# Kernel tuning notes

Hardware: AMD Instinct MI355X
Metric: run time of the kernel (lower is better)

The kernel has to match this reference:

```python
import jax, jax.numpy as jnp
import numpy as np
import math

D_MODEL = 512
N_HEADS = 8
D_K = D_MODEL // N_HEADS
B, S = 2, 4096
LN_EPS = 1e-5


def _xavier(key, fan_in, fan_out):
    limit = math.sqrt(6.0 / (fan_in + fan_out))
    return jax.random.uniform(key, (fan_in, fan_out), jnp.float32, -limit, limit)


def setup_inputs() -> dict:
    key = jax.random.key(0)
    ks = jax.random.split(key, 12)
    x = jax.random.normal(ks[0], (B, S, D_MODEL), jnp.float32)
    consciousness_state = jax.random.normal(ks[1], (B, D_MODEL), jnp.float32)
    # weights stored as [in, out] (equivalent to torch Linear weight.T)
    w_q = _xavier(ks[2], D_MODEL, D_MODEL)
    w_k = _xavier(ks[3], D_MODEL, D_MODEL)
    w_v = _xavier(ks[4], D_MODEL, D_MODEL)
    w_o = _xavier(ks[5], D_MODEL, D_MODEL)
    b_o = jnp.zeros((D_MODEL,), jnp.float32)
    w_gate = _xavier(ks[6], D_MODEL, N_HEADS)
    b_gate = jnp.zeros((N_HEADS,), jnp.float32)
    w_int = _xavier(ks[7], D_MODEL, D_MODEL)
    b_int = jnp.zeros((D_MODEL,), jnp.float32)
    ln_gamma = jnp.ones((D_MODEL,), jnp.float32)
    ln_beta = jnp.zeros((D_MODEL,), jnp.float32)
    return {"x": x, "consciousness_state": consciousness_state,
            "w_q": w_q, "w_k": w_k, "w_v": w_v, "w_o": w_o, "b_o": b_o,
            "w_gate": w_gate, "b_gate": b_gate, "w_int": w_int, "b_int": b_int,
            "ln_gamma": ln_gamma, "ln_beta": ln_beta}


def reference(x, consciousness_state, w_q, w_k, w_v, w_o, b_o,
              w_gate, b_gate, w_int, b_int, ln_gamma, ln_beta):
    b, s, d = x.shape
    # project and split heads: [B, H, S, d_k]
    def heads(w):
        return (x @ w).reshape(b, s, N_HEADS, D_K).transpose(0, 2, 1, 3)
    Q, K, V = heads(w_q), heads(w_k), heads(w_v)
    scores = jnp.einsum('bhsd,bhtd->bhst', Q, K) / math.sqrt(D_K)  # [B,H,S,S]
    # per-head consciousness gate BEFORE softmax
    cw = jax.nn.sigmoid(consciousness_state @ w_gate + b_gate)  # [B,H]
    scores = scores * cw[:, :, None, None]
    attn = jax.nn.softmax(scores, axis=-1)
    # dropout is identity in eval mode
    context = jnp.einsum('bhst,bhtd->bhsd', attn, V)
    context = context.transpose(0, 2, 1, 3).reshape(b, s, d)
    out = context @ w_o + b_o
    iw = jax.nn.sigmoid(consciousness_state @ w_int + b_int)  # [B,D]
    out = out * iw[:, None, :]
    # residual + LayerNorm
    h = out + x
    mu = jnp.mean(h, axis=-1, keepdims=True)
    var = jnp.var(h, axis=-1, keepdims=True)
    out = (h - mu) * jax.lax.rsqrt(var + LN_EPS) * ln_gamma + ln_beta
    return out, attn.mean(axis=1)
```

## Files before the change

### kernel.cpp

```cpp
#include <hip/hip_runtime.h>
#include <hip/hip_bf16.h>

using short8 = __attribute__((ext_vector_type(8))) short;
using f32x4  = __attribute__((ext_vector_type(4))) float;

#define S_LEN 4096
#define DM 512

__device__ __forceinline__ unsigned short f2b(float f) {
    unsigned int u = __float_as_uint(f);
    u += 0x7fffu + ((u >> 16) & 1u);
    return (unsigned short)(u >> 16);
}

__device__ __forceinline__ short8 pack8(float4 a, float4 b) {
    short8 r;
    r[0] = (short)f2b(a.x); r[1] = (short)f2b(a.y); r[2] = (short)f2b(a.z); r[3] = (short)f2b(a.w);
    r[4] = (short)f2b(b.x); r[5] = (short)f2b(b.y); r[6] = (short)f2b(b.z); r[7] = (short)f2b(b.w);
    return r;
}

__global__ __launch_bounds__(256) void convert_w(
    const float* __restrict__ w0, const float* __restrict__ w1,
    const float* __restrict__ w2, const float* __restrict__ w3,
    unsigned short* __restrict__ t0, unsigned short* __restrict__ t1,
    unsigned short* __restrict__ t2, unsigned short* __restrict__ t3)
{
    __shared__ float sh[64][65];
    const float* src; unsigned short* dst;
    switch (blockIdx.z) {
        case 0: src = w0; dst = t0; break;
        case 1: src = w1; dst = t1; break;
        case 2: src = w2; dst = t2; break;
        default: src = w3; dst = t3; break;
    }
    int k0 = blockIdx.x * 64, n0 = blockIdx.y * 64;
    int tid = threadIdx.x;
    for (int i = tid; i < 4096; i += 256) {
        int k = i >> 6, n = i & 63;
        sh[k][n] = src[(size_t)(k0 + k) * DM + n0 + n];
    }
    __syncthreads();
    for (int i = tid; i < 4096; i += 256) {
        int n = i >> 6, k = i & 63;
        dst[(size_t)(n0 + n) * DM + k0 + k] = f2b(sh[k][n]);
    }
}

__global__ __launch_bounds__(256) void convert_x(
    const float* __restrict__ x, unsigned short* __restrict__ xb)
{
    size_t i = ((size_t)blockIdx.x * 256 + threadIdx.x) * 8;
    float4 a = *reinterpret_cast<const float4*>(x + i);
    float4 b = *reinterpret_cast<const float4*>(x + i + 4);
    *reinterpret_cast<short8*>(xb + i) = pack8(a, b);
}

__global__ __launch_bounds__(64) void gates_kernel(
    const float* __restrict__ cs, const float* __restrict__ wg, const float* __restrict__ bg,
    const float* __restrict__ wi, const float* __restrict__ bi,
    float* __restrict__ cwout, float* __restrict__ iwout)
{
    int o = blockIdx.x, b = blockIdx.y, lane = threadIdx.x;
    const float* c = cs + (size_t)b * DM;
    float acc = 0.f;
    if (o < 8) {
        #pragma unroll
        for (int j = 0; j < 8; ++j) { int k = j * 64 + lane; acc += c[k] * wg[(size_t)k * 8 + o]; }
    } else {
        int n = o - 8;
        #pragma unroll
        for (int j = 0; j < 8; ++j) { int k = j * 64 + lane; acc += c[k] * wi[(size_t)k * DM + n]; }
    }
    #pragma unroll
    for (int d = 32; d; d >>= 1) acc += __shfl_xor(acc, d);
    if (lane == 0) {
        if (o < 8) cwout[b * 8 + o] = 1.f / (1.f + __expf(-(acc + bg[o])));
        else       iwout[b * DM + (o - 8)] = 1.f / (1.f + __expf(-(acc + bi[o - 8])));
    }
}

__global__ __launch_bounds__(256) void gemm_qkv(
    const unsigned short* __restrict__ A, const unsigned short* __restrict__ WT,
    const float* __restrict__ cw,
    unsigned short* __restrict__ Qb, unsigned short* __restrict__ Kb,
    unsigned short* __restrict__ Vt)
{
    __shared__ unsigned short a_sh[64][72];
    __shared__ unsigned short b_sh[64][72];
    const int m0 = blockIdx.x * 64;
    const int n0g = blockIdx.y * 64;
    const int which = blockIdx.y >> 3;
    const int tid = threadIdx.x;
    const int wave = tid >> 6, lane = tid & 63;
    const int g = lane >> 4, lr = lane & 15;
    const int srow = tid >> 3, skc = (tid & 7) * 8;

    float sq = 1.f;
    if (which == 0) {
        int b = blockIdx.x >> 6;
        int h = blockIdx.y & 7;
        sq = cw[b * 8 + h] * 0.125f * 1.44269504f;
    }

    f32x4 acc[4];
    #pragma unroll
    for (int i = 0; i < 4; ++i) acc[i] = (f32x4){0.f, 0.f, 0.f, 0.f};

    short8 ar[2], br[2];
    #pragma unroll
    for (int cc = 0; cc < 2; ++cc) {
        int row = srow + cc * 32;
        ar[cc] = *reinterpret_cast<const short8*>(A  + (size_t)(m0  + row) * DM + skc);
        br[cc] = *reinterpret_cast<const short8*>(WT + (size_t)(n0g + row) * DM + skc);
    }

    for (int k0 = 0; k0 < 512; k0 += 64) {
        #pragma unroll
        for (int cc = 0; cc < 2; ++cc) {
            int row = srow + cc * 32;
            *reinterpret_cast<short8*>(&a_sh[row][skc]) = ar[cc];
            *reinterpret_cast<short8*>(&b_sh[row][skc]) = br[cc];
        }
        __syncthreads();
        if (k0 + 64 < 512) {
            #pragma unroll
            for (int cc = 0; cc < 2; ++cc) {
                int row = srow + cc * 32;
                ar[cc] = *reinterpret_cast<const short8*>(A  + (size_t)(m0  + row) * DM + k0 + 64 + skc);
                br[cc] = *reinterpret_cast<const short8*>(WT + (size_t)(n0g + row) * DM + k0 + 64 + skc);
            }
        }
        __builtin_amdgcn_s_setprio(1);
        #pragma unroll
        for (int ks = 0; ks < 2; ++ks) {
            short8 af = *reinterpret_cast<const short8*>(&a_sh[wave * 16 + lr][ks * 32 + g * 8]);
            #pragma unroll
            for (int nf = 0; nf < 4; ++nf) {
                short8 bf = *reinterpret_cast<const short8*>(&b_sh[nf * 16 + lr][ks * 32 + g * 8]);
                acc[nf] = __builtin_amdgcn_mfma_f32_16x16x32_bf16(af, bf, acc[nf], 0, 0, 0);
            }
        }
        __builtin_amdgcn_s_setprio(0);
        __syncthreads();
    }

    #pragma unroll
    for (int nf = 0; nf < 4; ++nf) {
        #pragma unroll
        for (int r = 0; r < 4; ++r) {
            int m = m0 + wave * 16 + g * 4 + r;
            int nl = (blockIdx.y & 7) * 64 + nf * 16 + lr;
            unsigned short v = f2b(acc[nf][r] * sq);
            if (which == 0) {
                Qb[(size_t)m * DM + nl] = v;
            } else if (which == 1) {
                Kb[(size_t)m * DM + nl] = v;
            } else {
                int b = m >> 12, s = m & 4095;
                int h = nl >> 6, d = nl & 63;
                Vt[((size_t)(b * 8 + h) * 64 + d) * S_LEN + s] = v;
            }
        }
    }
}

__global__ __launch_bounds__(256) void gemm_proj(
    const unsigned short* __restrict__ A, const unsigned short* __restrict__ WT,
    float* __restrict__ outf, const float* __restrict__ bias,
    const float* __restrict__ iw, const float* __restrict__ xres)
{
    __shared__ unsigned short a_sh[64][72];
    __shared__ unsigned short b_sh[64][72];
    const int m0 = blockIdx.x * 64;
    const int n0 = blockIdx.y * 64;
    const int tid = threadIdx.x;
    const int wave = tid >> 6, lane = tid & 63;
    const int g = lane >> 4, lr = lane & 15;
    const int srow = tid >> 3, skc = (tid & 7) * 8;

    f32x4 acc[4];
    #pragma unroll
    for (int i = 0; i < 4; ++i) acc[i] = (f32x4){0.f, 0.f, 0.f, 0.f};

    short8 ar[2], br[2];
    #pragma unroll
    for (int cc = 0; cc < 2; ++cc) {
        int row = srow + cc * 32;
        ar[cc] = *reinterpret_cast<const short8*>(A  + (size_t)(m0 + row) * DM + skc);
        br[cc] = *reinterpret_cast<const short8*>(WT + (size_t)(n0 + row) * DM + skc);
    }

    for (int k0 = 0; k0 < 512; k0 += 64) {
        #pragma unroll
        for (int cc = 0; cc < 2; ++cc) {
            int row = srow + cc * 32;
            *reinterpret_cast<short8*>(&a_sh[row][skc]) = ar[cc];
            *reinterpret_cast<short8*>(&b_sh[row][skc]) = br[cc];
        }
        __syncthreads();
        if (k0 + 64 < 512) {
            #pragma unroll
            for (int cc = 0; cc < 2; ++cc) {
                int row = srow + cc * 32;
                ar[cc] = *reinterpret_cast<const short8*>(A  + (size_t)(m0 + row) * DM + k0 + 64 + skc);
                br[cc] = *reinterpret_cast<const short8*>(WT + (size_t)(n0 + row) * DM + k0 + 64 + skc);
            }
        }
        __builtin_amdgcn_s_setprio(1);
        #pragma unroll
        for (int ks = 0; ks < 2; ++ks) {
            short8 af = *reinterpret_cast<const short8*>(&a_sh[wave * 16 + lr][ks * 32 + g * 8]);
            #pragma unroll
            for (int nf = 0; nf < 4; ++nf) {
                short8 bf = *reinterpret_cast<const short8*>(&b_sh[nf * 16 + lr][ks * 32 + g * 8]);
                acc[nf] = __builtin_amdgcn_mfma_f32_16x16x32_bf16(af, bf, acc[nf], 0, 0, 0);
            }
        }
        __builtin_amdgcn_s_setprio(0);
        __syncthreads();
    }

    #pragma unroll
    for (int nf = 0; nf < 4; ++nf) {
        #pragma unroll
        for (int r = 0; r < 4; ++r) {
            int m = m0 + wave * 16 + g * 4 + r;
            int n = n0 + nf * 16 + lr;
            int b = m >> 12;
            float v = (acc[nf][r] + bias[n]) * iw[b * DM + n] + xres[(size_t)m * DM + n];
            outf[(size_t)m * DM + n] = v;
        }
    }
}

__global__ __launch_bounds__(256) void attn_ctx(
    const unsigned short* __restrict__ Qb, const unsigned short* __restrict__ Kb,
    const unsigned short* __restrict__ Vt,
    float* __restrict__ lbuf, unsigned short* __restrict__ ctx)
{
    __shared__ unsigned short k_sh[64][72];
    __shared__ unsigned short v_sh[64][72];
    __shared__ unsigned short p_sh[4][32][72];
    const int wg = blockIdx.x;
    const int logical = (wg & 7) * 64 + (wg >> 3);
    const int q0 = (logical & 31) * 128;
    const int bh = logical >> 5;
    const int b = bh >> 3, h = bh & 7;
    const int tid = threadIdx.x, wave = tid >> 6, lane = tid & 63;
    const int g = lane >> 4, lr = lane & 15;
    const int srow = tid >> 3, skc = (tid & 7) * 8;

    short8 qf[2][2];
    #pragma unroll
    for (int qq = 0; qq < 2; ++qq) {
        const unsigned short* qp = Qb + (size_t)(b * S_LEN + q0 + wave * 32 + qq * 16 + lr) * DM + h * 64;
        qf[qq][0] = *reinterpret_cast<const short8*>(qp + g * 8);
        qf[qq][1] = *reinterpret_cast<const short8*>(qp + 32 + g * 8);
    }
    short8 onesb;
    #pragma unroll
    for (int i = 0; i < 8; ++i) onesb[i] = (short)0x3F80;

    f32x4 lsum[2];
    f32x4 cacc[2][4];
    #pragma unroll
    for (int qq = 0; qq < 2; ++qq) {
        lsum[qq] = (f32x4){0.f, 0.f, 0.f, 0.f};
        #pragma unroll
        for (int i = 0; i < 4; ++i) cacc[qq][i] = (f32x4){0.f, 0.f, 0.f, 0.f};
    }

    const unsigned short* Kbase = Kb + (size_t)(b * S_LEN) * DM + h * 64;
    const unsigned short* Vbase = Vt + ((size_t)bh * 64) * S_LEN;

    short8 kr[2], vr[2];
    #pragma unroll
    for (int cc = 0; cc < 2; ++cc) {
        int row = srow + cc * 32;
        kr[cc] = *reinterpret_cast<const short8*>(Kbase + (size_t)row * DM + skc);
        vr[cc] = *reinterpret_cast<const short8*>(Vbase + (size_t)row * S_LEN + skc);
    }

    for (int kv0 = 0; kv0 < S_LEN; kv0 += 64) {
        #pragma unroll
        for (int cc = 0; cc < 2; ++cc) {
            int row = srow + cc * 32;
            *reinterpret_cast<short8*>(&k_sh[row][skc]) = kr[cc];
            *reinterpret_cast<short8*>(&v_sh[row][skc]) = vr[cc];
        }
        __syncthreads();
        f32x4 st[2][4];
        #pragma unroll
        for (int qq = 0; qq < 2; ++qq)
            #pragma unroll
            for (int f = 0; f < 4; ++f) st[qq][f] = (f32x4){0.f, 0.f, 0.f, 0.f};
        __builtin_amdgcn_s_setprio(1);
        #pragma unroll
        for (int ks = 0; ks < 2; ++ks) {
            #pragma unroll
            for (int f = 0; f < 4; ++f) {
                short8 kf = *reinterpret_cast<const short8*>(&k_sh[f * 16 + lr][ks * 32 + g * 8]);
                #pragma unroll
                for (int qq = 0; qq < 2; ++qq)
                    st[qq][f] = __builtin_amdgcn_mfma_f32_16x16x32_bf16(kf, qf[qq][ks], st[qq][f], 0, 0, 0);
            }
        }
        __builtin_amdgcn_s_setprio(0);
        if (kv0 + 64 < S_LEN) {
            #pragma unroll
            for (int cc = 0; cc < 2; ++cc) {
                int row = srow + cc * 32;
                kr[cc] = *reinterpret_cast<const short8*>(Kbase + (size_t)(kv0 + 64 + row) * DM + skc);
                vr[cc] = *reinterpret_cast<const short8*>(Vbase + (size_t)row * S_LEN + kv0 + 64 + skc);
            }
        }
        #pragma unroll
        for (int qq = 0; qq < 2; ++qq) {
            #pragma unroll
            for (int f = 0; f < 4; ++f) {
                float p0 = __builtin_amdgcn_exp2f(st[qq][f][0]);
                float p1 = __builtin_amdgcn_exp2f(st[qq][f][1]);
                float p2 = __builtin_amdgcn_exp2f(st[qq][f][2]);
                float p3 = __builtin_amdgcn_exp2f(st[qq][f][3]);
                unsigned u0, u1;
                asm("v_cvt_pk_bf16_f32 %0, %1, %2" : "=v"(u0) : "v"(p0), "v"(p1));
                asm("v_cvt_pk_bf16_f32 %0, %1, %2" : "=v"(u1) : "v"(p2), "v"(p3));
                uint2 pv; pv.x = u0; pv.y = u1;
                *reinterpret_cast<uint2*>(&p_sh[wave][qq * 16 + lr][f * 16 + g * 4]) = pv;
            }
        }
        __builtin_amdgcn_s_setprio(1);
        #pragma unroll
        for (int ks = 0; ks < 2; ++ks) {
            short8 pf[2];
            #pragma unroll
            for (int qq = 0; qq < 2; ++qq)
                pf[qq] = *reinterpret_cast<const short8*>(&p_sh[wave][qq * 16 + lr][ks * 32 + g * 8]);
            #pragma unroll
            for (int qq = 0; qq < 2; ++qq)
                lsum[qq] = __builtin_amdgcn_mfma_f32_16x16x32_bf16(pf[qq], onesb, lsum[qq], 0, 0, 0);
            #pragma unroll
            for (int df = 0; df < 4; ++df) {
                short8 vf = *reinterpret_cast<const short8*>(&v_sh[df * 16 + lr][ks * 32 + g * 8]);
                #pragma unroll
                for (int qq = 0; qq < 2; ++qq)
                    cacc[qq][df] = __builtin_amdgcn_mfma_f32_16x16x32_bf16(pf[qq], vf, cacc[qq][df], 0, 0, 0);
            }
        }
        __builtin_amdgcn_s_setprio(0);
        __syncthreads();
    }
    #pragma unroll
    for (int qq = 0; qq < 2; ++qq) {
        float rl[4];
        #pragma unroll
        for (int r = 0; r < 4; ++r) rl[r] = 1.f / lsum[qq][r];
        if (lr == 0) {
            #pragma unroll
            for (int r = 0; r < 4; ++r)
                lbuf[bh * S_LEN + q0 + wave * 32 + qq * 16 + g * 4 + r] = lsum[qq][r];
        }
        #pragma unroll
        for (int df = 0; df < 4; ++df) {
            #pragma unroll
            for (int r = 0; r < 4; ++r) {
                int q = q0 + wave * 32 + qq * 16 + g * 4 + r;
                ctx[(size_t)(b * S_LEN + q) * DM + h * 64 + df * 16 + lr] = f2b(cacc[qq][df][r] * rl[r]);
            }
        }
    }
}

__global__ __launch_bounds__(256) void attn_mean(
    const unsigned short* __restrict__ Qb, const unsigned short* __restrict__ Kb,
    const float* __restrict__ lbuf, float* __restrict__ outmean)
{
    __shared__ unsigned short k_sh[32][520];
    const int wg = blockIdx.x;
    const int logical = (wg & 7) * 128 + (wg >> 3);
    const int q0 = (logical & 63) * 64;
    const int kcb = logical >> 6;
    const int kc0 = (kcb & 7) * 512;
    const int b = kcb >> 3;
    const int tid = threadIdx.x, wave = tid >> 6, lane = tid & 63;
    const int g = lane >> 4, lr = lane & 15;
    const int srow = tid >> 6, scol = (tid & 63) * 8;

    float la2[8][4];
    #pragma unroll
    for (int h = 0; h < 8; ++h) {
        #pragma unroll
        for (int r = 0; r < 4; ++r) {
            int idx = (b * 8 + h) * S_LEN + q0 + wave * 16 + g * 4 + r;
            la2[h][r] = -log2f(lbuf[idx]) - 3.0f;
        }
    }
    const unsigned short* qbase = Qb + (size_t)(b * S_LEN + q0 + wave * 16 + lr) * DM;
    const unsigned short* Kbase = Kb + (size_t)(b * S_LEN) * DM;

    short8 stg[8];
    #pragma unroll
    for (int i = 0; i < 8; ++i) {
        int row = srow + i * 4;
        stg[i] = *reinterpret_cast<const short8*>(Kbase + (size_t)(kc0 + row) * DM + scol);
    }

    for (int t = 0; t < 16; ++t) {
        int kv0 = kc0 + t * 32;
        #pragma unroll
        for (int i = 0; i < 8; ++i) {
            int row = srow + i * 4;
            *reinterpret_cast<short8*>(&k_sh[row][scol]) = stg[i];
        }
        __syncthreads();
        if (t + 1 < 16) {
            #pragma unroll
            for (int i = 0; i < 8; ++i) {
                int row = srow + i * 4;
                stg[i] = *reinterpret_cast<const short8*>(Kbase + (size_t)(kv0 + 32 + row) * DM + scol);
            }
        }
        float macc[2][4];
        #pragma unroll
        for (int f = 0; f < 2; ++f)
            #pragma unroll
            for (int r = 0; r < 4; ++r) macc[f][r] = 0.f;
        #pragma unroll
        for (int h = 0; h < 8; ++h) {
            const unsigned short* qp = qbase + h * 64;
            short8 qf0 = *reinterpret_cast<const short8*>(qp + g * 8);
            short8 qf1 = *reinterpret_cast<const short8*>(qp + 32 + g * 8);
            f32x4 s[2];
            s[0] = (f32x4){0.f, 0.f, 0.f, 0.f};
            s[1] = (f32x4){0.f, 0.f, 0.f, 0.f};
            __builtin_amdgcn_s_setprio(1);
            #pragma unroll
            for (int f = 0; f < 2; ++f) {
                short8 kf0 = *reinterpret_cast<const short8*>(&k_sh[f * 16 + lr][h * 64 + g * 8]);
                s[f] = __builtin_amdgcn_mfma_f32_16x16x32_bf16(qf0, kf0, s[f], 0, 0, 0);
                short8 kf1 = *reinterpret_cast<const short8*>(&k_sh[f * 16 + lr][h * 64 + 32 + g * 8]);
                s[f] = __builtin_amdgcn_mfma_f32_16x16x32_bf16(qf1, kf1, s[f], 0, 0, 0);
            }
            __builtin_amdgcn_s_setprio(0);
            #pragma unroll
            for (int f = 0; f < 2; ++f)
                #pragma unroll
                for (int r = 0; r < 4; ++r)
                    macc[f][r] += __builtin_amdgcn_exp2f(s[f][r] + la2[h][r]);
        }
        #pragma unroll
        for (int f = 0; f < 2; ++f) {
            #pragma unroll
            for (int r = 0; r < 4; ++r) {
                int q = q0 + wave * 16 + g * 4 + r;
                outmean[(size_t)(b * S_LEN + q) * S_LEN + kv0 + f * 16 + lr] = macc[f][r];
            }
        }
        __syncthreads();
    }
}

__global__ __launch_bounds__(64) void ln_kernel(
    const float* __restrict__ hbuf, const float* __restrict__ gamma,
    const float* __restrict__ beta, float* __restrict__ dout)
{
    int row = blockIdx.x, lane = threadIdx.x;
    const float* hp = hbuf + (size_t)row * DM + lane * 8;
    float4 v0 = *reinterpret_cast<const float4*>(hp);
    float4 v1 = *reinterpret_cast<const float4*>(hp + 4);
    float s = v0.x + v0.y + v0.z + v0.w + v1.x + v1.y + v1.z + v1.w;
    float ss = v0.x * v0.x + v0.y * v0.y + v0.z * v0.z + v0.w * v0.w
             + v1.x * v1.x + v1.y * v1.y + v1.z * v1.z + v1.w * v1.w;
    #pragma unroll
    for (int d = 32; d; d >>= 1) { s += __shfl_xor(s, d); ss += __shfl_xor(ss, d); }
    float mu = s * (1.f / 512.f);
    float var = ss * (1.f / 512.f) - mu * mu;
    float rstd = rsqrtf(var + 1e-5f);
    float4 g0 = *reinterpret_cast<const float4*>(gamma + lane * 8);
    float4 g1 = *reinterpret_cast<const float4*>(gamma + lane * 8 + 4);
    float4 b0 = *reinterpret_cast<const float4*>(beta + lane * 8);
    float4 b1 = *reinterpret_cast<const float4*>(beta + lane * 8 + 4);
    float4 o0, o1;
    o0.x = (v0.x - mu) * rstd * g0.x + b0.x;
    o0.y = (v0.y - mu) * rstd * g0.y + b0.y;
    o0.z = (v0.z - mu) * rstd * g0.z + b0.z;
    o0.w = (v0.w - mu) * rstd * g0.w + b0.w;
    o1.x = (v1.x - mu) * rstd * g1.x + b1.x;
    o1.y = (v1.y - mu) * rstd * g1.y + b1.y;
    o1.z = (v1.z - mu) * rstd * g1.z + b1.z;
    o1.w = (v1.w - mu) * rstd * g1.w + b1.w;
    float* op = dout + (size_t)row * DM + lane * 8;
    *reinterpret_cast<float4*>(op) = o0;
    *reinterpret_cast<float4*>(op + 4) = o1;
}

extern "C" void kernel_launch(void* const* d_in, const int* in_sizes, int n_in,
                              void* d_out, int out_size, void* d_ws, size_t ws_size,
                              hipStream_t stream)
{
    const float* x   = (const float*)d_in[0];
    const float* cs  = (const float*)d_in[1];
    const float* wq  = (const float*)d_in[2];
    const float* wk  = (const float*)d_in[3];
    const float* wv  = (const float*)d_in[4];
    const float* wo  = (const float*)d_in[5];
    const float* bo  = (const float*)d_in[6];
    const float* wg  = (const float*)d_in[7];
    const float* bg  = (const float*)d_in[8];
    const float* wi  = (const float*)d_in[9];
    const float* bi  = (const float*)d_in[10];
    const float* gam = (const float*)d_in[11];
    const float* bet = (const float*)d_in[12];

    float* out = (float*)d_out;
    float* outmean = out + (size_t)2 * S_LEN * DM;

    char* ws = (char*)d_ws;
    size_t off = 0;
    auto alloc = [&](size_t bytes) { void* p = ws + off; off += (bytes + 255) & ~(size_t)255; return p; };

    unsigned short* wtq = (unsigned short*)alloc((size_t)DM * DM * 2);
    unsigned short* wtk = (unsigned short*)alloc((size_t)DM * DM * 2);
    unsigned short* wtv = (unsigned short*)alloc((size_t)DM * DM * 2);
    unsigned short* wto = (unsigned short*)alloc((size_t)DM * DM * 2);
    unsigned short* xb  = (unsigned short*)alloc((size_t)2 * S_LEN * DM * 2);
    unsigned short* Qb  = (unsigned short*)alloc((size_t)2 * S_LEN * DM * 2);
    unsigned short* Kb  = (unsigned short*)alloc((size_t)2 * S_LEN * DM * 2);
    unsigned short* Vt  = (unsigned short*)alloc((size_t)2 * S_LEN * DM * 2);
    unsigned short* ctx = (unsigned short*)alloc((size_t)2 * S_LEN * DM * 2);
    float* lbuf = (float*)alloc((size_t)16 * S_LEN * 4);
    float* cwb  = (float*)alloc(64);
    float* iwb  = (float*)alloc((size_t)2 * DM * 4);
    float* hbuf = (float*)Qb;

    convert_w<<<dim3(8, 8, 4), 256, 0, stream>>>(wq, wk, wv, wo, wtq, wtk, wtv, wto);
    convert_x<<<dim3(2048), 256, 0, stream>>>(x, xb);
    gates_kernel<<<dim3(520, 2), 64, 0, stream>>>(cs, wg, bg, wi, bi, cwb, iwb);

    gemm_qkv<<<dim3(128, 24), 256, 0, stream>>>(xb, wtq, cwb, Qb, Kb, Vt);

    attn_ctx<<<dim3(512), 256, 0, stream>>>(Qb, Kb, Vt, lbuf, ctx);
    attn_mean<<<dim3(1024), 256, 0, stream>>>(Qb, Kb, lbuf, outmean);

    gemm_proj<<<dim3(128, 8), 256, 0, stream>>>(ctx, wto, hbuf, bo, iwb, x);
    ln_kernel<<<dim3(2 * S_LEN), 64, 0, stream>>>(hbuf, gam, bet, out);
}
```

Before: 252.9 us.

## Split attention KV range across two workgroups and add combine kernel

The attention context kernel now splits the key/value sequence into two halves handled by separate workgroups, doubling the grid from 512 to 1024 blocks. Each block writes unnormalized fp32 partial context and row sums to a scratch buffer, and a new combine kernel adds the halves, normalizes, writes bf16 context and the row-sum buffer. The goal is better occupancy of the GPU's compute units, which 512 blocks did not fill well. In exchange it adds an extra launch and about 34 MB of fp32 scratch traffic. The combine is valid without max-rescaling because the softmax is computed without max subtraction.

Result: slower. 267.2 us (+5.6%).

```diff
diff --git a/kernel.cpp b/kernel.cpp
--- a/kernel.cpp
+++ b/kernel.cpp
@@ -236,17 +236,19 @@
 
 __global__ __launch_bounds__(256) void attn_ctx(
     const unsigned short* __restrict__ Qb, const unsigned short* __restrict__ Kb,
-    const unsigned short* __restrict__ Vt,
-    float* __restrict__ lbuf, unsigned short* __restrict__ ctx)
+    const unsigned short* __restrict__ Vt, float* __restrict__ pacc)
 {
     __shared__ unsigned short k_sh[64][72];
     __shared__ unsigned short v_sh[64][72];
     __shared__ unsigned short p_sh[4][32][72];
     const int wg = blockIdx.x;
-    const int logical = (wg & 7) * 64 + (wg >> 3);
-    const int q0 = (logical & 31) * 128;
-    const int bh = logical >> 5;
+    const int logical = (wg & 7) * 128 + (wg >> 3);
+    const int qt = logical & 31;
+    const int s = (logical >> 5) & 1;
+    const int bh = logical >> 6;
+    const int q0 = qt * 128;
     const int b = bh >> 3, h = bh & 7;
+    const int kvbeg = s * 2048, kvend = kvbeg + 2048;
     const int tid = threadIdx.x, wave = tid >> 6, lane = tid & 63;
     const int g = lane >> 4, lr = lane & 15;
     const int srow = tid >> 3, skc = (tid & 7) * 8;
@@ -278,11 +280,11 @@
     #pragma unroll
     for (int cc = 0; cc < 2; ++cc) {
         int row = srow + cc * 32;
-        kr[cc] = *reinterpret_cast<const short8*>(Kbase + (size_t)row * DM + skc);
-        vr[cc] = *reinterpret_cast<const short8*>(Vbase + (size_t)row * S_LEN + skc);
-    }
-
-    for (int kv0 = 0; kv0 < S_LEN; kv0 += 64) {
+        kr[cc] = *reinterpret_cast<const short8*>(Kbase + (size_t)(kvbeg + row) * DM + skc);
+        vr[cc] = *reinterpret_cast<const short8*>(Vbase + (size_t)row * S_LEN + kvbeg + skc);
+    }
+
+    for (int kv0 = kvbeg; kv0 < kvend; kv0 += 64) {
         #pragma unroll
         for (int cc = 0; cc < 2; ++cc) {
             int row = srow + cc * 32;
@@ -307,7 +309,7 @@
             }
         }
         __builtin_amdgcn_s_setprio(0);
-        if (kv0 + 64 < S_LEN) {
+        if (kv0 + 64 < kvend) {
             #pragma unroll
             for (int cc = 0; cc < 2; ++cc) {
                 int row = srow + cc * 32;
@@ -351,25 +353,52 @@
         __builtin_amdgcn_s_setprio(0);
         __syncthreads();
     }
+    float* pb = pacc + (size_t)logical * 8320;
     #pragma unroll
     for (int qq = 0; qq < 2; ++qq) {
-        float rl[4];
-        #pragma unroll
-        for (int r = 0; r < 4; ++r) rl[r] = 1.f / lsum[qq][r];
+        #pragma unroll
+        for (int df = 0; df < 4; ++df) {
+            #pragma unroll
+            for (int r = 0; r < 4; ++r)
+                pb[(wave * 32 + qq * 16 + g * 4 + r) * 64 + df * 16 + lr] = cacc[qq][df][r];
+        }
         if (lr == 0) {
             #pragma unroll
             for (int r = 0; r < 4; ++r)
-                lbuf[bh * S_LEN + q0 + wave * 32 + qq * 16 + g * 4 + r] = lsum[qq][r];
-        }
-        #pragma unroll
-        for (int df = 0; df < 4; ++df) {
-            #pragma unroll
-            for (int r = 0; r < 4; ++r) {
-                int q = q0 + wave * 32 + qq * 16 + g * 4 + r;
-                ctx[(size_t)(b * S_LEN + q) * DM + h * 64 + df * 16 + lr] = f2b(cacc[qq][df][r] * rl[r]);
-            }
-        }
-    }
+                pb[8192 + wave * 32 + qq * 16 + g * 4 + r] = lsum[qq][r];
+        }
+    }
+}
+
+__global__ __launch_bounds__(256) void attn_combine(
+    const float* __restrict__ pacc, float* __restrict__ lbuf,
+    unsigned short* __restrict__ ctx)
+{
+    const int L = blockIdx.x;
+    const int bh = L >> 6, c = L & 63;
+    const int b = bh >> 3, h = bh & 7;
+    const int qt = c >> 1, qh = c & 1;
+    const float* B0 = pacc + (size_t)(bh * 64 + qt) * 8320;
+    const float* B1 = pacc + (size_t)(bh * 64 + 32 + qt) * 8320;
+    const int tid = threadIdx.x;
+    const int q = tid >> 2, d0 = (tid & 3) * 16;
+    const int ql = qh * 64 + q;
+    float l = B0[8192 + ql] + B1[8192 + ql];
+    if ((tid & 3) == 0) lbuf[bh * S_LEN + qt * 128 + ql] = l;
+    float rl = 1.f / l;
+    unsigned short tmp[16];
+    #pragma unroll
+    for (int i = 0; i < 16; i += 4) {
+        float4 a0 = *reinterpret_cast<const float4*>(B0 + ql * 64 + d0 + i);
+        float4 a1 = *reinterpret_cast<const float4*>(B1 + ql * 64 + d0 + i);
+        tmp[i]     = f2b((a0.x + a1.x) * rl);
+        tmp[i + 1] = f2b((a0.y + a1.y) * rl);
+        tmp[i + 2] = f2b((a0.z + a1.z) * rl);
+        tmp[i + 3] = f2b((a0.w + a1.w) * rl);
+    }
+    unsigned short* cp = ctx + (size_t)(b * S_LEN + qt * 128 + ql) * DM + h * 64 + d0;
+    *reinterpret_cast<short8*>(cp)     = *reinterpret_cast<short8*>(tmp);
+    *reinterpret_cast<short8*>(cp + 8) = *reinterpret_cast<short8*>(tmp + 8);
 }
 
 __global__ __launch_bounds__(256) void attn_mean(
@@ -532,6 +561,7 @@
     float* lbuf = (float*)alloc((size_t)16 * S_LEN * 4);
     float* cwb  = (float*)alloc(64);
     float* iwb  = (float*)alloc((size_t)2 * DM * 4);
+    float* pacc = (float*)alloc((size_t)1024 * 8320 * 4);
     float* hbuf = (float*)Qb;
 
     convert_w<<<dim3(8, 8, 4), 256, 0, stream>>>(wq, wk, wv, wo, wtq, wtk, wtv, wto);
@@ -540,7 +570,8 @@
 
     gemm_qkv<<<dim3(128, 24), 256, 0, stream>>>(xb, wtq, cwb, Qb, Kb, Vt);
 
-    attn_ctx<<<dim3(512), 256, 0, stream>>>(Qb, Kb, Vt, lbuf, ctx);
+    attn_ctx<<<dim3(1024), 256, 0, stream>>>(Qb, Kb, Vt, pacc);
+    attn_combine<<<dim3(1024), 256, 0, stream>>>(pacc, lbuf, ctx);
     attn_mean<<<dim3(1024), 256, 0, stream>>>(Qb, Kb, lbuf, outmean);
 
     gemm_proj<<<dim3(128, 8), 256, 0, stream>>>(ctx, wto, hbuf, bo, iwb, x);
```
